# Kernel optimization log

Measured on AMD Instinct MI355X. Metric: run time of the kernel, lower is better.

Reference implementation:

```python
import jax, jax.numpy as jnp
import numpy as np

N_NODES = 100000
N_EDGES = 3200000
D_IN = 256
HID = 256
N_CLASSES = 40


def setup_inputs() -> dict:
    key = jax.random.key(0)
    k1, k2, k3, k4 = jax.random.split(key, 4)
    x = jax.random.normal(k1, (N_NODES, D_IN), dtype=jnp.float32)
    edge_index = jax.random.randint(k2, (2, N_EDGES), 0, N_NODES, dtype=jnp.int64)
    W1 = jax.random.normal(k3, (D_IN, HID), dtype=jnp.float32) * (1.0 / np.sqrt(D_IN))
    b1 = jnp.zeros((HID,), dtype=jnp.float32)
    W2 = jax.random.normal(k4, (HID, N_CLASSES), dtype=jnp.float32) * (1.0 / np.sqrt(HID))
    b2 = jnp.zeros((N_CLASSES,), dtype=jnp.float32)
    return {"x": x, "edge_index": edge_index, "W1": W1, "b1": b1, "W2": W2, "b2": b2}


def reference(x, edge_index, W1, b1, W2, b2):
    N = x.shape[0]
    loops = jnp.arange(N, dtype=edge_index.dtype)
    # gcn_norm: add self-loops, symmetric normalization D^-1/2 (A+I) D^-1/2
    src = jnp.concatenate([edge_index[0], loops])  # [E+N]
    dst = jnp.concatenate([edge_index[1], loops])
    ew = jnp.ones(src.shape[0], dtype=x.dtype)
    deg = jax.ops.segment_sum(ew, dst, num_segments=N)  # degree at target nodes
    dinv = jnp.where(deg > 0, jax.lax.rsqrt(deg), 0.0).astype(x.dtype)
    norm = dinv[src] * dinv[dst]  # [E+N]

    def propagate(h):
        # out[dst] += norm * h[src]  (SpMM via gather + segment scatter-add)
        return jax.ops.segment_sum(norm[:, None] * h[src], dst, num_segments=N)

    h = propagate(x) @ W1 + b1   # SGConv k=1 + Linear
    h = jax.nn.relu(h)
    h = propagate(h) @ W2 + b2
    return jax.nn.log_softmax(h, axis=1)
```

## Files before the change

### kernel.cpp

```cpp
#include <hip/hip_runtime.h>
#include <hip/hip_bf16.h>

#define N_NODES 100000
#define N_EDGES 3200000
#define D_IN 256
#define HID 256
#define NC 40
#define NBUCK 391
#define CHUNK 8192
#define BIN1_BLOCKS ((N_EDGES + CHUNK - 1) / CHUNK)
#define BCAP 16384
#define NPADE (NBUCK * BCAP)

typedef unsigned short u16;
typedef unsigned int u32;
typedef __attribute__((ext_vector_type(8))) short bf16x8;
typedef __attribute__((ext_vector_type(4))) float f32x4;
typedef __attribute__((ext_vector_type(2))) float f32x2;

static __device__ __forceinline__ float bf2f(u16 u) {
  union { unsigned int i; float f; } c; c.i = ((unsigned int)u) << 16; return c.f;
}
static __device__ __forceinline__ u16 f2bf(float f) {
  union { float f; unsigned int i; } c; c.f = f;
  unsigned int x = c.i;
  x += 0x7fffu + ((x >> 16) & 1u);
  return (u16)(x >> 16);
}

__global__ void k_zero(int* __restrict__ gcur) {
  int i = blockIdx.x * 256 + threadIdx.x;
  if (i < NBUCK) gcur[i] = i * BCAP;
}

__global__ __launch_bounds__(256) void k_bin1(const int* __restrict__ ei,
    int* __restrict__ gcur, u32* __restrict__ binned) {
  __shared__ int cnt[NBUCK];
  __shared__ int base[NBUCK];
  int t = threadIdx.x;
  int e0 = blockIdx.x * CHUNK;
  for (int j = t; j < NBUCK; j += 256) cnt[j] = 0;
  __syncthreads();
  for (int j = 0; j < CHUNK / 256; ++j) {
    int e = e0 + j * 256 + t;
    if (e < N_EDGES) {
      unsigned d = (unsigned)ei[N_EDGES + e];
      if (d < N_NODES) atomicAdd(&cnt[d >> 8], 1);
    }
  }
  __syncthreads();
  for (int j = t; j < NBUCK; j += 256)
    base[j] = cnt[j] ? atomicAdd(&gcur[j], cnt[j]) : 0;
  __syncthreads();
  for (int j = 0; j < CHUNK / 256; ++j) {
    int e = e0 + j * 256 + t;
    if (e < N_EDGES) {
      unsigned s = (unsigned)ei[e];
      unsigned d = (unsigned)ei[N_EDGES + e];
      if (s < N_NODES && d < N_NODES) {
        int b = d >> 8;
        int pos = atomicAdd(&base[b], 1);
        if ((unsigned)pos < NPADE)
          binned[pos] = ((d & 255u) << 17) | s;
      }
    }
  }
}

__global__ __launch_bounds__(256) void k_bin2(const u32* __restrict__ binned,
    const int* __restrict__ gcur, int* __restrict__ rp, int* __restrict__ re,
    float* __restrict__ dinv, int* __restrict__ ed) {
  __shared__ int cnt[256];
  __shared__ int s[256];
  __shared__ int cur[256];
  int b = blockIdx.x, t = threadIdx.x;
  int start = b * BCAP, end = gcur[b];
  cnt[t] = 0;
  __syncthreads();
  for (int i = start + t; i < end; i += 256)
    atomicAdd(&cnt[binned[i] >> 17], 1);
  __syncthreads();
  int v = cnt[t];
  s[t] = v;
  __syncthreads();
  for (int off = 1; off < 256; off <<= 1) {
    int add = (t >= off) ? s[t - off] : 0;
    __syncthreads();
    s[t] += add;
    __syncthreads();
  }
  int excl = s[t] - v;
  int n = b * 256 + t;
  if (n < N_NODES) {
    rp[n] = start + excl;
    re[n] = start + excl + v;
    dinv[n] = rsqrtf((float)v + 1.0f);
  }
  cur[t] = start + excl;
  __syncthreads();
  for (int i = start + t; i < end; i += 256) {
    u32 rec = binned[i];
    int pos = atomicAdd(&cur[rec >> 17], 1);
    if ((unsigned)pos < NPADE) ed[pos] = (int)(rec & 0x1FFFFu);
  }
}

__global__ void k_w1t(const float* __restrict__ W1, u16* __restrict__ w1t) {
  int n = blockIdx.x, k = threadIdx.x;
  w1t[n * 256 + k] = f2bf(W1[k * 256 + n]);
}
__global__ void k_w2t(const float* __restrict__ W2, u16* __restrict__ w2t) {
  int n = blockIdx.x, k = threadIdx.x;
  w2t[n * 256 + k] = (n < NC) ? f2bf(W2[k * NC + n]) : (u16)0;
}

__global__ __launch_bounds__(256) void k_gemm1(const float* __restrict__ x,
    const u16* __restrict__ w1t, const float* __restrict__ dinv,
    unsigned char* __restrict__ y) {
  __shared__ char smem[20480];
  short* sA = (short*)smem;
  short* sB = (short*)(smem + 10240);
  float* sdinv = (float*)(smem + 18432);
  int tid = threadIdx.x;
  int wave = tid >> 6, lane = tid & 63;
  int lq = lane >> 4, lr = lane & 15;
  int wm = (wave >> 1) * 64, wn = (wave & 1) * 64;
  int row0 = blockIdx.y * 128;
  int col0 = blockIdx.x * 128;
  int sr = tid >> 1;
  int sh = (tid & 1) * 16;
  int arow = row0 + sr;
  bool aval = arow < N_NODES;
  const float* axf = x + (size_t)arow * 256 + sh;
  const u16* bx = w1t + (size_t)(col0 + sr) * 256 + sh;
  f32x4 acc[4][4] = {};
  for (int k0 = 0; k0 < 256; k0 += 32) {
    float4 f0 = {}, f1 = {}, f2 = {}, f3 = {};
    if (aval) {
      f0 = *(const float4*)(axf + k0);
      f1 = *(const float4*)(axf + k0 + 4);
      f2 = *(const float4*)(axf + k0 + 8);
      f3 = *(const float4*)(axf + k0 + 12);
    }
    uint4 vb0 = *(const uint4*)(bx + k0);
    uint4 vb1 = *(const uint4*)(bx + k0 + 8);
    uint4 pa0, pa1;
    pa0.x = (u32)f2bf(f0.x) | ((u32)f2bf(f0.y) << 16);
    pa0.y = (u32)f2bf(f0.z) | ((u32)f2bf(f0.w) << 16);
    pa0.z = (u32)f2bf(f1.x) | ((u32)f2bf(f1.y) << 16);
    pa0.w = (u32)f2bf(f1.z) | ((u32)f2bf(f1.w) << 16);
    pa1.x = (u32)f2bf(f2.x) | ((u32)f2bf(f2.y) << 16);
    pa1.y = (u32)f2bf(f2.z) | ((u32)f2bf(f2.w) << 16);
    pa1.z = (u32)f2bf(f3.x) | ((u32)f2bf(f3.y) << 16);
    pa1.w = (u32)f2bf(f3.z) | ((u32)f2bf(f3.w) << 16);
    __syncthreads();
    *(uint4*)&sA[sr * 40 + sh] = pa0;
    *(uint4*)&sA[sr * 40 + sh + 8] = pa1;
    *(uint4*)&sB[sr * 40 + sh] = vb0;
    *(uint4*)&sB[sr * 40 + sh + 8] = vb1;
    __syncthreads();
    bf16x8 af[4], bfr[4];
#pragma unroll
    for (int mt = 0; mt < 4; ++mt)
      af[mt] = *(const bf16x8*)&sA[(wm + mt * 16 + lr) * 40 + lq * 8];
#pragma unroll
    for (int nt = 0; nt < 4; ++nt)
      bfr[nt] = *(const bf16x8*)&sB[(wn + nt * 16 + lr) * 40 + lq * 8];
#pragma unroll
    for (int mt = 0; mt < 4; ++mt)
#pragma unroll
      for (int nt = 0; nt < 4; ++nt)
        acc[mt][nt] = __builtin_amdgcn_mfma_f32_16x16x32_bf16(
            af[mt], bfr[nt], acc[mt][nt], 0, 0, 0);
  }
  __syncthreads();
  if (tid < 128) {
    int rr = row0 + tid;
    sdinv[tid] = (rr < N_NODES) ? dinv[rr] : 0.f;
  }
  __syncthreads();
#pragma unroll
  for (int mt = 0; mt < 4; ++mt)
#pragma unroll
    for (int nt = 0; nt < 4; ++nt) {
      int c = wn + nt * 16 + lr;
#pragma unroll
      for (int i = 0; i < 4; ++i) {
        int r = wm + mt * 16 + lq * 4 + i;
        float sv = sdinv[r] * acc[mt][nt][i];
        int pk = __builtin_amdgcn_cvt_pk_fp8_f32(sv, sv, 0, false);
        smem[r * 144 + c] = (char)(pk & 0xFF);
      }
    }
  __syncthreads();
  if (aval) {
    unsigned char* dst = y + (size_t)arow * 256 + col0 + (tid & 1) * 64;
    const char* srcp = smem + sr * 144 + (tid & 1) * 64;
#pragma unroll
    for (int j = 0; j < 4; ++j)
      ((uint4*)dst)[j] = *(const uint4*)(srcp + j * 16);
  }
}

#define ACC8(U) do { \
    acc[0] += __builtin_amdgcn_cvt_pk_f32_fp8((U).x, false); \
    acc[1] += __builtin_amdgcn_cvt_pk_f32_fp8((U).x, true);  \
    acc[2] += __builtin_amdgcn_cvt_pk_f32_fp8((U).y, false); \
    acc[3] += __builtin_amdgcn_cvt_pk_f32_fp8((U).y, true);  \
    acc[4] += __builtin_amdgcn_cvt_pk_f32_fp8((U).z, false); \
    acc[5] += __builtin_amdgcn_cvt_pk_f32_fp8((U).z, true);  \
    acc[6] += __builtin_amdgcn_cvt_pk_f32_fp8((U).w, false); \
    acc[7] += __builtin_amdgcn_cvt_pk_f32_fp8((U).w, true);  \
  } while (0)

__global__ __launch_bounds__(256) void k_spmm1(const uint4* __restrict__ y16,
    const int* __restrict__ ed, const int* __restrict__ rp,
    const int* __restrict__ re, const float* __restrict__ dinv,
    const float* __restrict__ b1, u16* __restrict__ h1) {
  int lane = threadIdx.x & 63;
  int row = (blockIdx.x << 2) + (threadIdx.x >> 6);
  int g = lane >> 4, p = lane & 15;
  float di = dinv[row];
  uint4 sv = y16[(size_t)row * 16 + p];
  f32x2 acc[8];
  f32x2 z2 = {0.f, 0.f};
  if (g == 0) {
    acc[0] = __builtin_amdgcn_cvt_pk_f32_fp8(sv.x, false);
    acc[1] = __builtin_amdgcn_cvt_pk_f32_fp8(sv.x, true);
    acc[2] = __builtin_amdgcn_cvt_pk_f32_fp8(sv.y, false);
    acc[3] = __builtin_amdgcn_cvt_pk_f32_fp8(sv.y, true);
    acc[4] = __builtin_amdgcn_cvt_pk_f32_fp8(sv.z, false);
    acc[5] = __builtin_amdgcn_cvt_pk_f32_fp8(sv.z, true);
    acc[6] = __builtin_amdgcn_cvt_pk_f32_fp8(sv.w, false);
    acc[7] = __builtin_amdgcn_cvt_pk_f32_fp8(sv.w, true);
  } else {
#pragma unroll
    for (int i = 0; i < 8; ++i) acc[i] = z2;
  }
  int e = rp[row], e1 = re[row];
  if (e + 16 <= e1) {
    int s0 = ed[e + g], s1 = ed[e + 4 + g];
    int s2 = ed[e + 8 + g], s3 = ed[e + 12 + g];
    while (true) {
      uint4 u0 = y16[(size_t)s0 * 16 + p];
      uint4 u1 = y16[(size_t)s1 * 16 + p];
      uint4 u2 = y16[(size_t)s2 * 16 + p];
      uint4 u3 = y16[(size_t)s3 * 16 + p];
      e += 16;
      bool more = (e + 16 <= e1);
      if (more) {
        s0 = ed[e + g]; s1 = ed[e + 4 + g];
        s2 = ed[e + 8 + g]; s3 = ed[e + 12 + g];
      }
      ACC8(u0);
      ACC8(u1);
      ACC8(u2);
      ACC8(u3);
      if (!more) break;
    }
  }
  for (; e + 4 <= e1; e += 4) {
    int s0 = ed[e + g];
    uint4 u0 = y16[(size_t)s0 * 16 + p];
    ACC8(u0);
  }
  int rem = e1 - e;
  if (rem > 0) {
    int s0 = ed[e + (g < rem ? g : 0)];
    uint4 u0 = y16[(size_t)s0 * 16 + p];
    if (g < rem) ACC8(u0);
  }
#pragma unroll
  for (int i = 0; i < 8; ++i) {
    acc[i].x += __shfl_xor(acc[i].x, 16);
    acc[i].y += __shfl_xor(acc[i].y, 16);
    acc[i].x += __shfl_xor(acc[i].x, 32);
    acc[i].y += __shfl_xor(acc[i].y, 32);
  }
  if (g == 0) {
    const float4* bb4 = (const float4*)(b1 + p * 16);
    u16 o[16];
#pragma unroll
    for (int i = 0; i < 4; ++i) {
      float4 bb = bb4[i];
      float a0 = fmaxf(di * acc[2 * i].x + bb.x, 0.f);
      float a1 = fmaxf(di * acc[2 * i].y + bb.y, 0.f);
      float a2 = fmaxf(di * acc[2 * i + 1].x + bb.z, 0.f);
      float a3 = fmaxf(di * acc[2 * i + 1].y + bb.w, 0.f);
      o[4 * i + 0] = f2bf(a0);
      o[4 * i + 1] = f2bf(a1);
      o[4 * i + 2] = f2bf(a2);
      o[4 * i + 3] = f2bf(a3);
    }
    u16* dst = h1 + (size_t)row * HID + p * 16;
    *(uint4*)dst = *(const uint4*)&o[0];
    *(uint4*)(dst + 8) = *(const uint4*)&o[8];
  }
}

__global__ __launch_bounds__(256) void k_gemm2(const u16* __restrict__ h1,
    const u16* __restrict__ w2t, const float* __restrict__ dinv,
    u16* __restrict__ zbp) {
  __shared__ char smem[16384];
  short* sA = (short*)smem;
  short* sB = (short*)(smem + 10240);
  float* sdinv = (float*)(smem + 14336);
  u16* sC = (u16*)smem;
  int tid = threadIdx.x;
  int wave = tid >> 6, lane = tid & 63;
  int lq = lane >> 4, lr = lane & 15;
  int wm = wave * 32;
  int row0 = blockIdx.x * 128;
  int sr = tid >> 1;
  int sh = (tid & 1) * 16;
  int arow = row0 + sr;
  bool aval = arow < N_NODES;
  const u16* ax = h1 + (size_t)arow * 256 + sh;
  int br = tid >> 1;
  const u16* bx = w2t + (size_t)br * 256 + sh;
  if (tid < 128) {
    int rr = row0 + tid;
    sdinv[tid] = (rr < N_NODES) ? dinv[rr] : 0.f;
  }
  f32x4 acc[2][3] = {};
  for (int k0 = 0; k0 < 256; k0 += 32) {
    uint4 a0 = {}, a1 = {};
    if (aval) {
      a0 = *(const uint4*)(ax + k0);
      a1 = *(const uint4*)(ax + k0 + 8);
    }
    uint4 b0 = {}, b1v = {};
    if (tid < 96) {
      b0 = *(const uint4*)(bx + k0);
      b1v = *(const uint4*)(bx + k0 + 8);
    }
    __syncthreads();
    *(uint4*)&sA[sr * 40 + sh] = a0;
    *(uint4*)&sA[sr * 40 + sh + 8] = a1;
    if (tid < 96) {
      *(uint4*)&sB[br * 40 + sh] = b0;
      *(uint4*)&sB[br * 40 + sh + 8] = b1v;
    }
    __syncthreads();
    bf16x8 af[2], bfr[3];
#pragma unroll
    for (int mt = 0; mt < 2; ++mt)
      af[mt] = *(const bf16x8*)&sA[(wm + mt * 16 + lr) * 40 + lq * 8];
#pragma unroll
    for (int nt = 0; nt < 3; ++nt)
      bfr[nt] = *(const bf16x8*)&sB[(nt * 16 + lr) * 40 + lq * 8];
#pragma unroll
    for (int mt = 0; mt < 2; ++mt)
#pragma unroll
      for (int nt = 0; nt < 3; ++nt)
        acc[mt][nt] = __builtin_amdgcn_mfma_f32_16x16x32_bf16(
            af[mt], bfr[nt], acc[mt][nt], 0, 0, 0);
  }
  __syncthreads();
#pragma unroll
  for (int mt = 0; mt < 2; ++mt)
#pragma unroll
    for (int nt = 0; nt < 3; ++nt) {
      int c = nt * 16 + lr;
#pragma unroll
      for (int i = 0; i < 4; ++i) {
        int r = wm + mt * 16 + lq * 4 + i;
        sC[r * 56 + c] = f2bf(sdinv[r] * acc[mt][nt][i]);
      }
    }
  __syncthreads();
  if (tid < 128) {
    int orow = row0 + tid;
    if (orow < N_NODES) {
      u16* dst = zbp + (size_t)orow * 64;
#pragma unroll
      for (int j = 0; j < 6; ++j)
        ((uint4*)dst)[j] = *(const uint4*)&sC[tid * 56 + j * 8];
      uint4 z = {};
      ((uint4*)dst)[6] = z;
      ((uint4*)dst)[7] = z;
    }
  }
}

#define ZACC(U) do { \
    acc[0] += __uint_as_float((U).x << 16); \
    acc[1] += __uint_as_float((U).x & 0xFFFF0000u); \
    acc[2] += __uint_as_float((U).y << 16); \
    acc[3] += __uint_as_float((U).y & 0xFFFF0000u); \
    acc[4] += __uint_as_float((U).z << 16); \
    acc[5] += __uint_as_float((U).z & 0xFFFF0000u); \
    acc[6] += __uint_as_float((U).w << 16); \
    acc[7] += __uint_as_float((U).w & 0xFFFF0000u); \
  } while (0)

__global__ __launch_bounds__(256) void k_spmm2(const uint4* __restrict__ zb4,
    const int* __restrict__ ed, const int* __restrict__ rp,
    const int* __restrict__ re, const float* __restrict__ dinv,
    const float* __restrict__ b2, float* __restrict__ out) {
  int lane = threadIdx.x & 63;
  int row = (blockIdx.x << 2) + (threadIdx.x >> 6);
  int g = lane >> 3, p = lane & 7;
  float di = dinv[row];
  float acc[8];
  uint4 sv = zb4[(size_t)row * 8 + p];
  if (g == 0) {
    acc[0] = __uint_as_float(sv.x << 16);
    acc[1] = __uint_as_float(sv.x & 0xFFFF0000u);
    acc[2] = __uint_as_float(sv.y << 16);
    acc[3] = __uint_as_float(sv.y & 0xFFFF0000u);
    acc[4] = __uint_as_float(sv.z << 16);
    acc[5] = __uint_as_float(sv.z & 0xFFFF0000u);
    acc[6] = __uint_as_float(sv.w << 16);
    acc[7] = __uint_as_float(sv.w & 0xFFFF0000u);
  } else {
#pragma unroll
    for (int i = 0; i < 8; ++i) acc[i] = 0.f;
  }
  int e = rp[row], e1 = re[row];
  if (e + 32 <= e1) {
    int s0 = ed[e + g], s1 = ed[e + 8 + g];
    int s2 = ed[e + 16 + g], s3 = ed[e + 24 + g];
    while (true) {
      uint4 u0 = zb4[(size_t)s0 * 8 + p];
      uint4 u1 = zb4[(size_t)s1 * 8 + p];
      uint4 u2 = zb4[(size_t)s2 * 8 + p];
      uint4 u3 = zb4[(size_t)s3 * 8 + p];
      e += 32;
      bool more = (e + 32 <= e1);
      if (more) {
        s0 = ed[e + g]; s1 = ed[e + 8 + g];
        s2 = ed[e + 16 + g]; s3 = ed[e + 24 + g];
      }
      ZACC(u0);
      ZACC(u1);
      ZACC(u2);
      ZACC(u3);
      if (!more) break;
    }
  }
  for (; e + 8 <= e1; e += 8) {
    int s0 = ed[e + g];
    uint4 u0 = zb4[(size_t)s0 * 8 + p];
    ZACC(u0);
  }
  int rem = e1 - e;
  if (g < rem) {
    int s0 = ed[e + g];
    uint4 u0 = zb4[(size_t)s0 * 8 + p];
    ZACC(u0);
  }
#pragma unroll
  for (int i = 0; i < 8; ++i) {
    acc[i] += __shfl_xor(acc[i], 8);
    acc[i] += __shfl_xor(acc[i], 16);
    acc[i] += __shfl_xor(acc[i], 32);
  }
  bool valid = p < 5;
  float val[8];
  if (valid) {
    float4 bb0 = *(const float4*)(b2 + p * 8);
    float4 bb1 = *(const float4*)(b2 + p * 8 + 4);
    val[0] = di * acc[0] + bb0.x;
    val[1] = di * acc[1] + bb0.y;
    val[2] = di * acc[2] + bb0.z;
    val[3] = di * acc[3] + bb0.w;
    val[4] = di * acc[4] + bb1.x;
    val[5] = di * acc[5] + bb1.y;
    val[6] = di * acc[6] + bb1.z;
    val[7] = di * acc[7] + bb1.w;
  } else {
#pragma unroll
    for (int i = 0; i < 8; ++i) val[i] = 0.f;
  }
  float mv = -3.0e38f;
  if (valid) {
#pragma unroll
    for (int i = 0; i < 8; ++i) mv = fmaxf(mv, val[i]);
  }
  mv = fmaxf(mv, __shfl_xor(mv, 1));
  mv = fmaxf(mv, __shfl_xor(mv, 2));
  mv = fmaxf(mv, __shfl_xor(mv, 4));
  float sum = 0.f;
  if (valid) {
#pragma unroll
    for (int i = 0; i < 8; ++i) sum += expf(val[i] - mv);
  }
  sum += __shfl_xor(sum, 1);
  sum += __shfl_xor(sum, 2);
  sum += __shfl_xor(sum, 4);
  float ls = logf(sum);
  if (g == 0 && valid) {
    float4 o0, o1;
    o0.x = val[0] - mv - ls; o0.y = val[1] - mv - ls;
    o0.z = val[2] - mv - ls; o0.w = val[3] - mv - ls;
    o1.x = val[4] - mv - ls; o1.y = val[5] - mv - ls;
    o1.z = val[6] - mv - ls; o1.w = val[7] - mv - ls;
    float* dst = out + (size_t)row * NC + p * 8;
    *(float4*)dst = o0;
    *(float4*)(dst + 4) = o1;
  }
}

extern "C" void kernel_launch(void* const* d_in, const int* in_sizes, int n_in,
                              void* d_out, int out_size, void* d_ws, size_t ws_size,
                              hipStream_t stream) {
  const float* x  = (const float*)d_in[0];
  const int*   ei = (const int*)d_in[1];
  const float* W1 = (const float*)d_in[2];
  const float* b1 = (const float*)d_in[3];
  const float* W2 = (const float*)d_in[4];
  const float* b2 = (const float*)d_in[5];
  float* out = (float*)d_out;

  char* ws = (char*)d_ws;
  size_t off = 0;
  auto alloc = [&](size_t bytes) {
    char* p = ws + off;
    off = (off + bytes + 255) & ~(size_t)255;
    return p;
  };
  int*   gcur   = (int*)  alloc((size_t)NBUCK * 4);
  int*   rp     = (int*)  alloc((size_t)N_NODES * 4);
  int*   re     = (int*)  alloc((size_t)N_NODES * 4);
  float* dinv   = (float*)alloc((size_t)N_NODES * 4);
  u32*   binned = (u32*)  alloc((size_t)NPADE * 4);
  int*   ed     = (int*)  alloc((size_t)NPADE * 4);
  unsigned char* y = (unsigned char*)alloc((size_t)N_NODES * 256);
  u16*   w1t    = (u16*)  alloc((size_t)256 * 256 * 2);
  u16*   w2t    = (u16*)  alloc((size_t)48 * 256 * 2);
  u16*   h1     = (u16*)  alloc((size_t)N_NODES * HID * 2);
  u16*   zbp    = (u16*)  alloc((size_t)N_NODES * 64 * 2);

  k_zero<<<2, 256, 0, stream>>>(gcur);
  k_bin1<<<BIN1_BLOCKS, 256, 0, stream>>>(ei, gcur, binned);
  k_bin2<<<NBUCK, 256, 0, stream>>>(binned, gcur, rp, re, dinv, ed);
  k_w1t<<<256, 256, 0, stream>>>(W1, w1t);
  k_w2t<<<48, 256, 0, stream>>>(W2, w2t);
  k_gemm1<<<dim3(2, (N_NODES + 127) / 128), 256, 0, stream>>>(x, w1t, dinv, y);
  k_spmm1<<<N_NODES / 4, 256, 0, stream>>>((const uint4*)y, ed, rp, re, dinv, b1, h1);
  k_gemm2<<<(N_NODES + 127) / 128, 256, 0, stream>>>(h1, w2t, dinv, zbp);
  k_spmm2<<<N_NODES / 4, 256, 0, stream>>>((const uint4*)zbp, ed, rp, re, dinv, b2, out);
}
```

Measured before the change: 492.8 us.

## Split first SpMM into column-slab sweeps with slab-major fp8 layout

The first GEMM now writes its fp8 output in 32-column slabs stored slab-major. The first SpMM is then launched once per slab, so each sweep's random gathers hit a small working set that can stay in cache. The cost is re-reading the edge and row-pointer arrays once per sweep, extra kernel launches, and narrower 8-byte gathers per lane.

```diff
diff --git a/kernel.cpp b/kernel.cpp
--- a/kernel.cpp
+++ b/kernel.cpp
@@ -11,6 +11,7 @@
 #define BIN1_BLOCKS ((N_EDGES + CHUNK - 1) / CHUNK)
 #define BCAP 16384
 #define NPADE (NBUCK * BCAP)
+#define NSWEEP 8
 
 typedef unsigned short u16;
 typedef unsigned int u32;
@@ -194,107 +195,96 @@
     }
   __syncthreads();
   if (aval) {
-    unsigned char* dst = y + (size_t)arow * 256 + col0 + (tid & 1) * 64;
+    int colbase = col0 + (tid & 1) * 64;
     const char* srcp = smem + sr * 144 + (tid & 1) * 64;
 #pragma unroll
-    for (int j = 0; j < 4; ++j)
-      ((uint4*)dst)[j] = *(const uint4*)(srcp + j * 16);
-  }
-}
-
-#define ACC8(U) do { \
+    for (int j = 0; j < 4; ++j) {
+      int col = colbase + j * 16;
+      unsigned char* dst = y +
+          ((size_t)(col >> 5) * N_NODES + arow) * 32 + (col & 31);
+      *(uint4*)dst = *(const uint4*)(srcp + j * 16);
+    }
+  }
+}
+
+#define ACC4(U) do { \
     acc[0] += __builtin_amdgcn_cvt_pk_f32_fp8((U).x, false); \
     acc[1] += __builtin_amdgcn_cvt_pk_f32_fp8((U).x, true);  \
     acc[2] += __builtin_amdgcn_cvt_pk_f32_fp8((U).y, false); \
     acc[3] += __builtin_amdgcn_cvt_pk_f32_fp8((U).y, true);  \
-    acc[4] += __builtin_amdgcn_cvt_pk_f32_fp8((U).z, false); \
-    acc[5] += __builtin_amdgcn_cvt_pk_f32_fp8((U).z, true);  \
-    acc[6] += __builtin_amdgcn_cvt_pk_f32_fp8((U).w, false); \
-    acc[7] += __builtin_amdgcn_cvt_pk_f32_fp8((U).w, true);  \
   } while (0)
 
-__global__ __launch_bounds__(256) void k_spmm1(const uint4* __restrict__ y16,
+__global__ __launch_bounds__(256) void k_spmm1(const unsigned char* __restrict__ y,
     const int* __restrict__ ed, const int* __restrict__ rp,
     const int* __restrict__ re, const float* __restrict__ dinv,
-    const float* __restrict__ b1, u16* __restrict__ h1) {
+    const float* __restrict__ b1, u16* __restrict__ h1, int c) {
   int lane = threadIdx.x & 63;
   int row = (blockIdx.x << 2) + (threadIdx.x >> 6);
-  int g = lane >> 4, p = lane & 15;
+  int g = lane >> 2, p = lane & 3;
+  const uint2* yc = (const uint2*)(y + (size_t)c * N_NODES * 32);
   float di = dinv[row];
-  uint4 sv = y16[(size_t)row * 16 + p];
-  f32x2 acc[8];
+  f32x2 acc[4];
   f32x2 z2 = {0.f, 0.f};
+  uint2 sv = yc[(size_t)row * 4 + p];
   if (g == 0) {
     acc[0] = __builtin_amdgcn_cvt_pk_f32_fp8(sv.x, false);
     acc[1] = __builtin_amdgcn_cvt_pk_f32_fp8(sv.x, true);
     acc[2] = __builtin_amdgcn_cvt_pk_f32_fp8(sv.y, false);
     acc[3] = __builtin_amdgcn_cvt_pk_f32_fp8(sv.y, true);
-    acc[4] = __builtin_amdgcn_cvt_pk_f32_fp8(sv.z, false);
-    acc[5] = __builtin_amdgcn_cvt_pk_f32_fp8(sv.z, true);
-    acc[6] = __builtin_amdgcn_cvt_pk_f32_fp8(sv.w, false);
-    acc[7] = __builtin_amdgcn_cvt_pk_f32_fp8(sv.w, true);
   } else {
 #pragma unroll
-    for (int i = 0; i < 8; ++i) acc[i] = z2;
+    for (int i = 0; i < 4; ++i) acc[i] = z2;
   }
   int e = rp[row], e1 = re[row];
-  if (e + 16 <= e1) {
-    int s0 = ed[e + g], s1 = ed[e + 4 + g];
-    int s2 = ed[e + 8 + g], s3 = ed[e + 12 + g];
+  if (e + 32 <= e1) {
+    int s0 = ed[e + g], s1 = ed[e + 16 + g];
     while (true) {
-      uint4 u0 = y16[(size_t)s0 * 16 + p];
-      uint4 u1 = y16[(size_t)s1 * 16 + p];
-      uint4 u2 = y16[(size_t)s2 * 16 + p];
-      uint4 u3 = y16[(size_t)s3 * 16 + p];
-      e += 16;
-      bool more = (e + 16 <= e1);
-      if (more) {
-        s0 = ed[e + g]; s1 = ed[e + 4 + g];
-        s2 = ed[e + 8 + g]; s3 = ed[e + 12 + g];
-      }
-      ACC8(u0);
-      ACC8(u1);
-      ACC8(u2);
-      ACC8(u3);
+      uint2 u0 = yc[(size_t)s0 * 4 + p];
+      uint2 u1 = yc[(size_t)s1 * 4 + p];
+      e += 32;
+      bool more = (e + 32 <= e1);
+      if (more) { s0 = ed[e + g]; s1 = ed[e + 16 + g]; }
+      ACC4(u0);
+      ACC4(u1);
       if (!more) break;
     }
   }
-  for (; e + 4 <= e1; e += 4) {
+  for (; e + 16 <= e1; e += 16) {
     int s0 = ed[e + g];
-    uint4 u0 = y16[(size_t)s0 * 16 + p];
-    ACC8(u0);
+    uint2 u0 = yc[(size_t)s0 * 4 + p];
+    ACC4(u0);
   }
   int rem = e1 - e;
   if (rem > 0) {
     int s0 = ed[e + (g < rem ? g : 0)];
-    uint4 u0 = y16[(size_t)s0 * 16 + p];
-    if (g < rem) ACC8(u0);
-  }
-#pragma unroll
-  for (int i = 0; i < 8; ++i) {
+    uint2 u0 = yc[(size_t)s0 * 4 + p];
+    if (g < rem) ACC4(u0);
+  }
+#pragma unroll
+  for (int i = 0; i < 4; ++i) {
+    acc[i].x += __shfl_xor(acc[i].x, 4);
+    acc[i].y += __shfl_xor(acc[i].y, 4);
+    acc[i].x += __shfl_xor(acc[i].x, 8);
+    acc[i].y += __shfl_xor(acc[i].y, 8);
     acc[i].x += __shfl_xor(acc[i].x, 16);
     acc[i].y += __shfl_xor(acc[i].y, 16);
     acc[i].x += __shfl_xor(acc[i].x, 32);
     acc[i].y += __shfl_xor(acc[i].y, 32);
   }
   if (g == 0) {
-    const float4* bb4 = (const float4*)(b1 + p * 16);
-    u16 o[16];
-#pragma unroll
-    for (int i = 0; i < 4; ++i) {
-      float4 bb = bb4[i];
-      float a0 = fmaxf(di * acc[2 * i].x + bb.x, 0.f);
-      float a1 = fmaxf(di * acc[2 * i].y + bb.y, 0.f);
-      float a2 = fmaxf(di * acc[2 * i + 1].x + bb.z, 0.f);
-      float a3 = fmaxf(di * acc[2 * i + 1].y + bb.w, 0.f);
-      o[4 * i + 0] = f2bf(a0);
-      o[4 * i + 1] = f2bf(a1);
-      o[4 * i + 2] = f2bf(a2);
-      o[4 * i + 3] = f2bf(a3);
-    }
-    u16* dst = h1 + (size_t)row * HID + p * 16;
-    *(uint4*)dst = *(const uint4*)&o[0];
-    *(uint4*)(dst + 8) = *(const uint4*)&o[8];
+    const float* bb = b1 + c * 32 + p * 8;
+    float4 bb0 = *(const float4*)bb;
+    float4 bb1 = *(const float4*)(bb + 4);
+    u16 o[8];
+    o[0] = f2bf(fmaxf(di * acc[0].x + bb0.x, 0.f));
+    o[1] = f2bf(fmaxf(di * acc[0].y + bb0.y, 0.f));
+    o[2] = f2bf(fmaxf(di * acc[1].x + bb0.z, 0.f));
+    o[3] = f2bf(fmaxf(di * acc[1].y + bb0.w, 0.f));
+    o[4] = f2bf(fmaxf(di * acc[2].x + bb1.x, 0.f));
+    o[5] = f2bf(fmaxf(di * acc[2].y + bb1.y, 0.f));
+    o[6] = f2bf(fmaxf(di * acc[3].x + bb1.z, 0.f));
+    o[7] = f2bf(fmaxf(di * acc[3].y + bb1.w, 0.f));
+    *(uint4*)(h1 + (size_t)row * HID + c * 32 + p * 8) = *(const uint4*)&o[0];
   }
 }
 
@@ -538,7 +528,8 @@
   k_w1t<<<256, 256, 0, stream>>>(W1, w1t);
   k_w2t<<<48, 256, 0, stream>>>(W2, w2t);
   k_gemm1<<<dim3(2, (N_NODES + 127) / 128), 256, 0, stream>>>(x, w1t, dinv, y);
-  k_spmm1<<<N_NODES / 4, 256, 0, stream>>>((const uint4*)y, ed, rp, re, dinv, b1, h1);
+  for (int c = 0; c < NSWEEP; ++c)
+    k_spmm1<<<N_NODES / 4, 256, 0, stream>>>(y, ed, rp, re, dinv, b1, h1, c);
   k_gemm2<<<(N_NODES + 127) / 128, 256, 0, stream>>>(h1, w2t, dinv, zbp);
   k_spmm2<<<N_NODES / 4, 256, 0, stream>>>((const uint4*)zbp, ed, rp, re, dinv, b2, out);
 }
```

New measurement: 738.5 us. 49.9% more time.

## Replace bucketed two-pass binning with global degree count, scan and atomic scatter

Applied to the files above, without the earlier changes.

CSR construction no longer bins edges into fixed-capacity destination buckets through a staging array. It now counts per-node degree with global atomics, builds offsets with a three-kernel scan, and scatters source ids straight into a compact edge array. This removes the padded bucket buffer and its second pass, but uses global atomics on node counters and launches more small kernels. The SpMM kernels are also each split into two launches over half the rows, which looks like a probe or a bid for cache locality.

```diff
diff --git a/kernel.cpp b/kernel.cpp
--- a/kernel.cpp
+++ b/kernel.cpp
@@ -6,11 +6,7 @@
 #define D_IN 256
 #define HID 256
 #define NC 40
-#define NBUCK 391
-#define CHUNK 8192
-#define BIN1_BLOCKS ((N_EDGES + CHUNK - 1) / CHUNK)
-#define BCAP 16384
-#define NPADE (NBUCK * BCAP)
+#define SCAN_B 391
 
 typedef unsigned short u16;
 typedef unsigned int u32;
@@ -28,80 +24,87 @@
   return (u16)(x >> 16);
 }
 
-__global__ void k_zero(int* __restrict__ gcur) {
+__global__ __launch_bounds__(256) void k_zdeg(int* __restrict__ deg) {
   int i = blockIdx.x * 256 + threadIdx.x;
-  if (i < NBUCK) gcur[i] = i * BCAP;
-}
-
-__global__ __launch_bounds__(256) void k_bin1(const int* __restrict__ ei,
-    int* __restrict__ gcur, u32* __restrict__ binned) {
-  __shared__ int cnt[NBUCK];
-  __shared__ int base[NBUCK];
+  if (i < N_NODES) deg[i] = 0;
+}
+
+__global__ __launch_bounds__(256) void k_deg(const int* __restrict__ ei,
+    int* __restrict__ deg) {
+  int e = blockIdx.x * 256 + threadIdx.x;
+  if (e < N_EDGES) {
+    unsigned s = (unsigned)ei[e];
+    unsigned d = (unsigned)ei[N_EDGES + e];
+    if (s < N_NODES && d < N_NODES) atomicAdd(&deg[d], 1);
+  }
+}
+
+__global__ __launch_bounds__(256) void k_scan1(const int* __restrict__ deg,
+    int* __restrict__ bt) {
+  __shared__ int s[256];
+  int b = blockIdx.x, t = threadIdx.x;
+  int n = b * 256 + t;
+  int v = (n < N_NODES) ? deg[n] : 0;
+  s[t] = v;
+  __syncthreads();
+  for (int off = 1; off < 256; off <<= 1) {
+    int a = (t >= off) ? s[t - off] : 0;
+    __syncthreads();
+    s[t] += a;
+    __syncthreads();
+  }
+  if (t == 255) bt[b] = s[255];
+}
+
+__global__ void k_scan2(const int* __restrict__ bt, int* __restrict__ btoff) {
+  __shared__ int s[512];
   int t = threadIdx.x;
-  int e0 = blockIdx.x * CHUNK;
-  for (int j = t; j < NBUCK; j += 256) cnt[j] = 0;
-  __syncthreads();
-  for (int j = 0; j < CHUNK / 256; ++j) {
-    int e = e0 + j * 256 + t;
-    if (e < N_EDGES) {
-      unsigned d = (unsigned)ei[N_EDGES + e];
-      if (d < N_NODES) atomicAdd(&cnt[d >> 8], 1);
-    }
-  }
-  __syncthreads();
-  for (int j = t; j < NBUCK; j += 256)
-    base[j] = cnt[j] ? atomicAdd(&gcur[j], cnt[j]) : 0;
-  __syncthreads();
-  for (int j = 0; j < CHUNK / 256; ++j) {
-    int e = e0 + j * 256 + t;
-    if (e < N_EDGES) {
-      unsigned s = (unsigned)ei[e];
-      unsigned d = (unsigned)ei[N_EDGES + e];
-      if (s < N_NODES && d < N_NODES) {
-        int b = d >> 8;
-        int pos = atomicAdd(&base[b], 1);
-        if ((unsigned)pos < NPADE)
-          binned[pos] = ((d & 255u) << 17) | s;
-      }
-    }
-  }
-}
-
-__global__ __launch_bounds__(256) void k_bin2(const u32* __restrict__ binned,
-    const int* __restrict__ gcur, int* __restrict__ rp, int* __restrict__ re,
-    float* __restrict__ dinv, int* __restrict__ ed) {
-  __shared__ int cnt[256];
+  int v = (t < SCAN_B) ? bt[t] : 0;
+  s[t] = v;
+  __syncthreads();
+  for (int off = 1; off < 512; off <<= 1) {
+    int a = (t >= off) ? s[t - off] : 0;
+    __syncthreads();
+    s[t] += a;
+    __syncthreads();
+  }
+  if (t < SCAN_B) btoff[t] = s[t] - v;
+}
+
+__global__ __launch_bounds__(256) void k_scan3(const int* __restrict__ deg,
+    const int* __restrict__ btoff, int* __restrict__ rp, int* __restrict__ re,
+    float* __restrict__ dinv, int* __restrict__ cur) {
   __shared__ int s[256];
-  __shared__ int cur[256];
   int b = blockIdx.x, t = threadIdx.x;
-  int start = b * BCAP, end = gcur[b];
-  cnt[t] = 0;
-  __syncthreads();
-  for (int i = start + t; i < end; i += 256)
-    atomicAdd(&cnt[binned[i] >> 17], 1);
-  __syncthreads();
-  int v = cnt[t];
+  int n = b * 256 + t;
+  int v = (n < N_NODES) ? deg[n] : 0;
   s[t] = v;
   __syncthreads();
   for (int off = 1; off < 256; off <<= 1) {
-    int add = (t >= off) ? s[t - off] : 0;
-    __syncthreads();
-    s[t] += add;
-    __syncthreads();
-  }
-  int excl = s[t] - v;
-  int n = b * 256 + t;
+    int a = (t >= off) ? s[t - off] : 0;
+    __syncthreads();
+    s[t] += a;
+    __syncthreads();
+  }
   if (n < N_NODES) {
-    rp[n] = start + excl;
-    re[n] = start + excl + v;
+    int excl = btoff[b] + s[t] - v;
+    rp[n] = excl;
+    re[n] = excl + v;
     dinv[n] = rsqrtf((float)v + 1.0f);
-  }
-  cur[t] = start + excl;
-  __syncthreads();
-  for (int i = start + t; i < end; i += 256) {
-    u32 rec = binned[i];
-    int pos = atomicAdd(&cur[rec >> 17], 1);
-    if ((unsigned)pos < NPADE) ed[pos] = (int)(rec & 0x1FFFFu);
+    cur[n] = excl;
+  }
+}
+
+__global__ __launch_bounds__(256) void k_scat(const int* __restrict__ ei,
+    int* __restrict__ cur, int* __restrict__ ed) {
+  int e = blockIdx.x * 256 + threadIdx.x;
+  if (e < N_EDGES) {
+    unsigned s = (unsigned)ei[e];
+    unsigned d = (unsigned)ei[N_EDGES + e];
+    if (s < N_NODES && d < N_NODES) {
+      int pos = atomicAdd(&cur[d], 1);
+      ed[pos] = (int)s;
+    }
   }
 }
 
@@ -216,9 +219,9 @@
 __global__ __launch_bounds__(256) void k_spmm1(const uint4* __restrict__ y16,
     const int* __restrict__ ed, const int* __restrict__ rp,
     const int* __restrict__ re, const float* __restrict__ dinv,
-    const float* __restrict__ b1, u16* __restrict__ h1) {
+    const float* __restrict__ b1, u16* __restrict__ h1, int row0) {
   int lane = threadIdx.x & 63;
-  int row = (blockIdx.x << 2) + (threadIdx.x >> 6);
+  int row = row0 + (blockIdx.x << 2) + (threadIdx.x >> 6);
   int g = lane >> 4, p = lane & 15;
   float di = dinv[row];
   uint4 sv = y16[(size_t)row * 16 + p];
@@ -397,9 +400,9 @@
 __global__ __launch_bounds__(256) void k_spmm2(const uint4* __restrict__ zb4,
     const int* __restrict__ ed, const int* __restrict__ rp,
     const int* __restrict__ re, const float* __restrict__ dinv,
-    const float* __restrict__ b2, float* __restrict__ out) {
+    const float* __restrict__ b2, float* __restrict__ out, int row0) {
   int lane = threadIdx.x & 63;
-  int row = (blockIdx.x << 2) + (threadIdx.x >> 6);
+  int row = row0 + (blockIdx.x << 2) + (threadIdx.x >> 6);
   int g = lane >> 3, p = lane & 7;
   float di = dinv[row];
   float acc[8];
@@ -520,25 +523,32 @@
     off = (off + bytes + 255) & ~(size_t)255;
     return p;
   };
-  int*   gcur   = (int*)  alloc((size_t)NBUCK * 4);
+  int*   deg    = (int*)  alloc((size_t)N_NODES * 4);
+  int*   bt     = (int*)  alloc((size_t)SCAN_B * 4);
+  int*   btoff  = (int*)  alloc((size_t)SCAN_B * 4);
   int*   rp     = (int*)  alloc((size_t)N_NODES * 4);
   int*   re     = (int*)  alloc((size_t)N_NODES * 4);
+  int*   cur    = (int*)  alloc((size_t)N_NODES * 4);
   float* dinv   = (float*)alloc((size_t)N_NODES * 4);
-  u32*   binned = (u32*)  alloc((size_t)NPADE * 4);
-  int*   ed     = (int*)  alloc((size_t)NPADE * 4);
+  int*   ed     = (int*)  alloc((size_t)N_EDGES * 4);
   unsigned char* y = (unsigned char*)alloc((size_t)N_NODES * 256);
   u16*   w1t    = (u16*)  alloc((size_t)256 * 256 * 2);
   u16*   w2t    = (u16*)  alloc((size_t)48 * 256 * 2);
   u16*   h1     = (u16*)  alloc((size_t)N_NODES * HID * 2);
   u16*   zbp    = (u16*)  alloc((size_t)N_NODES * 64 * 2);
 
-  k_zero<<<2, 256, 0, stream>>>(gcur);
-  k_bin1<<<BIN1_BLOCKS, 256, 0, stream>>>(ei, gcur, binned);
-  k_bin2<<<NBUCK, 256, 0, stream>>>(binned, gcur, rp, re, dinv, ed);
+  k_zdeg<<<SCAN_B, 256, 0, stream>>>(deg);
+  k_deg<<<(N_EDGES + 255) / 256, 256, 0, stream>>>(ei, deg);
+  k_scan1<<<SCAN_B, 256, 0, stream>>>(deg, bt);
+  k_scan2<<<1, 512, 0, stream>>>(bt, btoff);
+  k_scan3<<<SCAN_B, 256, 0, stream>>>(deg, btoff, rp, re, dinv, cur);
+  k_scat<<<(N_EDGES + 255) / 256, 256, 0, stream>>>(ei, cur, ed);
   k_w1t<<<256, 256, 0, stream>>>(W1, w1t);
   k_w2t<<<48, 256, 0, stream>>>(W2, w2t);
   k_gemm1<<<dim3(2, (N_NODES + 127) / 128), 256, 0, stream>>>(x, w1t, dinv, y);
-  k_spmm1<<<N_NODES / 4, 256, 0, stream>>>((const uint4*)y, ed, rp, re, dinv, b1, h1);
+  k_spmm1<<<N_NODES / 8, 256, 0, stream>>>((const uint4*)y, ed, rp, re, dinv, b1, h1, 0);
+  k_spmm1<<<N_NODES / 8, 256, 0, stream>>>((const uint4*)y, ed, rp, re, dinv, b1, h1, N_NODES / 2);
   k_gemm2<<<(N_NODES + 127) / 128, 256, 0, stream>>>(h1, w2t, dinv, zbp);
-  k_spmm2<<<N_NODES / 4, 256, 0, stream>>>((const uint4*)zbp, ed, rp, re, dinv, b2, out);
-}
+  k_spmm2<<<N_NODES / 8, 256, 0, stream>>>((const uint4*)zbp, ed, rp, re, dinv, b2, out, 0);
+  k_spmm2<<<N_NODES / 8, 256, 0, stream>>>((const uint4*)zbp, ed, rp, re, dinv, b2, out, N_NODES / 2);
+}
```

After: 798.7 us. +62.1%, slower.
